# Optimization experiments

Measured on AMD Instinct MI355X. Metric: run time of the kernel, lower is better.

Reference implementation:

```python
import jax, jax.numpy as jnp
import numpy as np

DIM = 256
N_EMBED = 8192
DECAY = 0.99
EPS = 1e-05


def setup_inputs() -> dict:
    key = jax.random.key(0)
    k1, k2, k3, k4 = jax.random.split(key, 4)
    z = jax.random.normal(k1, (16, 32, 32, DIM), dtype=jnp.float32)
    embedding = jax.random.normal(k2, (DIM, N_EMBED), dtype=jnp.float32)
    cluster_size = jax.random.uniform(k3, (N_EMBED,), dtype=jnp.float32)
    embedding_avg = jax.random.normal(k4, (DIM, N_EMBED), dtype=jnp.float32)
    return {"z": z, "embedding": embedding, "cluster_size": cluster_size,
            "embedding_avg": embedding_avg}


def reference(z, embedding, cluster_size, embedding_avg):
    flatten = z.reshape(-1, DIM)  # [N, dim]
    dist = ((flatten ** 2).sum(1, keepdims=True)
            - 2.0 * flatten @ embedding
            + (embedding ** 2).sum(0, keepdims=True))
    embed_ind_flat = jnp.argmin(dist, axis=1)  # [N] int
    embed_ind = embed_ind_flat.reshape(z.shape[:-1])
    # Gather codes: embedding is [dim, n_embed]; quantize [..., dim]
    quantize = jnp.take(embedding.T, embed_ind_flat, axis=0).reshape(z.shape)

    # EMA codebook update (training path), via segment sums (no dense one-hot)
    onehot_sum = jax.ops.segment_sum(
        jnp.ones_like(embed_ind_flat, dtype=flatten.dtype),
        embed_ind_flat, num_segments=N_EMBED)  # [n_embed]
    embed_sum = jax.ops.segment_sum(flatten, embed_ind_flat,
                                    num_segments=N_EMBED).T  # [dim, n_embed]
    new_cluster_size = cluster_size * DECAY + (1.0 - DECAY) * onehot_sum
    new_embedding_avg = embedding_avg * DECAY + (1.0 - DECAY) * embed_sum
    n = new_cluster_size.sum()
    smoothed = (new_cluster_size + EPS) / (n + N_EMBED * EPS) * n
    new_embedding = new_embedding_avg / smoothed[None, :]

    diff = jnp.mean((jax.lax.stop_gradient(quantize) - z) ** 2)
    quantize_st = z + jax.lax.stop_gradient(quantize - z)
    return (quantize_st, diff, embed_ind, new_embedding,
            new_cluster_size, new_embedding_avg)
```

## Files before the change

### kernel.cpp

```cpp
#include <hip/hip_runtime.h>


#define DIMC  256
#define NEMB  8192
#define NROWS 16384

#define OUT_Q      0u
#define OUT_DIFF   4194304u
#define OUT_IDX    4194305u
#define OUT_NEWEMB 4210689u
#define OUT_NEWCS  6307841u
#define OUT_NEWAVG 6316033u

#define WS_EHI    0u
#define WS_ELO    1048576u
#define WS_COUNT  2097152u
#define WS_DIFF   2105344u
#define WS_N      2105345u
#define WS_ENORM  2105346u
#define WS_PACK   2113540u

typedef __attribute__((ext_vector_type(8))) short short8;
typedef __attribute__((ext_vector_type(4))) float f32x4;

__device__ inline void split_bf16(float x, unsigned short& h, unsigned short& l) {
  unsigned u = __float_as_uint(x);
  unsigned r = u + 0x7FFFu + ((u >> 16) & 1u);
  h = (unsigned short)(r >> 16);
  float hf = __uint_as_float((unsigned)h << 16);
  float lo = x - hf;
  unsigned u2 = __float_as_uint(lo);
  unsigned r2 = u2 + 0x7FFFu + ((u2 >> 16) & 1u);
  l = (unsigned short)(r2 >> 16);
}

__device__ inline float bf16_f(unsigned short u) {
  return __uint_as_float((unsigned)u << 16);
}

__global__ __launch_bounds__(256) void prep_kernel(
    const float* __restrict__ z, const float* __restrict__ emb,
    const float* __restrict__ cs, unsigned short* __restrict__ z_hi,
    unsigned short* __restrict__ z_lo, unsigned short* __restrict__ e_hi,
    unsigned short* __restrict__ e_lo, float* __restrict__ enorm,
    float* __restrict__ embsum, unsigned long long* __restrict__ pack,
    float* __restrict__ count_diff, float* __restrict__ n_out) {
  const int b = blockIdx.x;
  const int t = threadIdx.x;
  __shared__ float tile[64][68];
  __shared__ float red[4][64];

  if (b < 1024) {
#pragma unroll
    for (int it = 0; it < 4; ++it) {
      const int idx = (b * 256 + t) + it * 262144;
      const float4 v = reinterpret_cast<const float4*>(z)[idx];
      ushort4 h, l;
      split_bf16(v.x, h.x, l.x);
      split_bf16(v.y, h.y, l.y);
      split_bf16(v.z, h.z, l.z);
      split_bf16(v.w, h.w, l.w);
      reinterpret_cast<ushort4*>(z_hi)[idx] = h;
      reinterpret_cast<ushort4*>(z_lo)[idx] = l;
    }
  } else if (b < 1536) {
    const int bb = b - 1024;
    const int n0 = (bb & 127) * 64;
    const int k0 = (bb >> 7) * 64;
    const int c4 = (t & 15) * 4;
    const int rr = t >> 4;
#pragma unroll
    for (int i = 0; i < 4; ++i) {
      const int kl = rr + i * 16;
      const float4 v = *reinterpret_cast<const float4*>(
          &emb[(size_t)(k0 + kl) * NEMB + n0 + c4]);
      *reinterpret_cast<float4*>(&tile[kl][c4]) = v;
    }
    __syncthreads();
#pragma unroll
    for (int i = 0; i < 4; ++i) {
      const int nr = rr + i * 16;
      float4 v;
      v.x = tile[c4 + 0][nr];
      v.y = tile[c4 + 1][nr];
      v.z = tile[c4 + 2][nr];
      v.w = tile[c4 + 3][nr];
      const size_t off = (size_t)(n0 + nr) * DIMC + k0 + c4;
      ushort4 h, l;
      split_bf16(v.x, h.x, l.x);
      split_bf16(v.y, h.y, l.y);
      split_bf16(v.z, h.z, l.z);
      split_bf16(v.w, h.w, l.w);
      *reinterpret_cast<ushort4*>(&e_hi[off]) = h;
      *reinterpret_cast<ushort4*>(&e_lo[off]) = l;
    }
  } else if (b < 2048) {
    const int bb = b - 1536;
    const float4 zero = {0.f, 0.f, 0.f, 0.f};
#pragma unroll
    for (int it = 0; it < 4; ++it)
      reinterpret_cast<float4*>(embsum)[bb * 1024 + t + it * 256] = zero;
  } else if (b < 2176) {
    const int l = t & 63;
    const int dg = t >> 6;
    const int e = (b - 2048) * 64 + l;
    float s = 0.f;
#pragma unroll 8
    for (int d = dg * 64; d < dg * 64 + 64; ++d) {
      const float v = emb[(size_t)d * NEMB + e];
      s = fmaf(v, v, s);
    }
    red[dg][l] = s;
    __syncthreads();
    if (dg == 0) enorm[e] = red[0][l] + red[1][l] + red[2][l] + red[3][l];
  } else if (b < 2184) {
    const int bb = b - 2176;
    const uint4 ff = {~0u, ~0u, ~0u, ~0u};
#pragma unroll
    for (int it = 0; it < 4; ++it)
      reinterpret_cast<uint4*>(pack)[bb * 1024 + t + it * 256] = ff;
  } else if (b == 2184) {
    for (int i = t; i < 8193; i += 256) count_diff[i] = 0.f;
  } else {
    float s = 0.f;
#pragma unroll
    for (int i = 0; i < 32; ++i) s += cs[t + i * 256];
#pragma unroll
    for (int off = 32; off > 0; off >>= 1) s += __shfl_down(s, off, 64);
    if ((t & 63) == 0) red[0][t >> 6] = s;
    __syncthreads();
    if (t == 0)
      n_out[0] = 0.99f * (red[0][0] + red[0][1] + red[0][2] + red[0][3]) +
                 163.84f;
  }
}

__global__ __launch_bounds__(256, 2) void argmin_mfma_kernel(
    const unsigned short* __restrict__ z_hi, const unsigned short* __restrict__ z_lo,
    const unsigned short* __restrict__ e_hi, const unsigned short* __restrict__ e_lo,
    const float* __restrict__ enorm, unsigned long long* __restrict__ pack) {
  __shared__ short za[16384];
  __shared__ short eb[16384];
  const int tid = threadIdx.x;
  const int bid = blockIdx.x;
  const int r0 = (bid >> 2) * 128;
  const int ebase = (bid & 3) * 2048;
  const int tx = tid & 15;
  const int q = (tid >> 4) & 3;
  const int wave = tid >> 6;
  const int wm = wave & 1;
  const int wn = wave >> 1;

  float rmin[4][4];
  int ridx[4][4];
#pragma unroll
  for (int i = 0; i < 4; ++i)
#pragma unroll
    for (int r = 0; r < 4; ++r) { rmin[i][r] = 3.4028235e38f; ridx[i][r] = 0; }

  for (int nt = 0; nt < 16; ++nt) {
    const int n0 = ebase + nt * 128;
    f32x4 acc[4][4];
#pragma unroll
    for (int i = 0; i < 4; ++i)
#pragma unroll
      for (int j = 0; j < 4; ++j) acc[i][j] = (f32x4)0.0f;

    for (int kt = 0; kt < 4; ++kt) {
      const int k0 = kt * 64;
      __syncthreads();
#pragma unroll
      for (int it = 0; it < 8; ++it) {
        const int P = tid + it * 256;
        const int row = P >> 4;
        const int p = P & 15;
        const int o = (p & 7) ^ (row & 7);
        const unsigned short* zsrc =
            ((p & 8) ? z_lo : z_hi) + (size_t)(r0 + row) * DIMC + k0 + o * 8;
        __builtin_amdgcn_global_load_lds(
            (const __attribute__((address_space(1))) unsigned int*)zsrc,
            (__attribute__((address_space(3))) unsigned int*)&za[P * 8], 16, 0, 0);
        const unsigned short* esrc =
            ((p & 8) ? e_lo : e_hi) + (size_t)(n0 + row) * DIMC + k0 + o * 8;
        __builtin_amdgcn_global_load_lds(
            (const __attribute__((address_space(1))) unsigned int*)esrc,
            (__attribute__((address_space(3))) unsigned int*)&eb[P * 8], 16, 0, 0);
      }
      __syncthreads();
#pragma unroll
      for (int ks = 0; ks < 2; ++ks) {
        short8 ah[4], al[4], bh[4], bl[4];
#pragma unroll
        for (int i = 0; i < 4; ++i) {
          const int rl = wm * 64 + i * 16 + tx;
          const int oa = (ks * 4 + q) ^ (rl & 7);
          ah[i] = *reinterpret_cast<const short8*>(&za[rl * 128 + oa * 8]);
          al[i] = *reinterpret_cast<const short8*>(&za[rl * 128 + (oa + 8) * 8]);
          const int cl = wn * 64 + i * 16 + tx;
          const int ob = (ks * 4 + q) ^ (cl & 7);
          bh[i] = *reinterpret_cast<const short8*>(&eb[cl * 128 + ob * 8]);
          bl[i] = *reinterpret_cast<const short8*>(&eb[cl * 128 + (ob + 8) * 8]);
        }
#pragma unroll
        for (int i = 0; i < 4; ++i)
#pragma unroll
          for (int j = 0; j < 4; ++j) {
            acc[i][j] = __builtin_amdgcn_mfma_f32_16x16x32_bf16(ah[i], bh[j],
                                                               acc[i][j], 0, 0, 0);
            acc[i][j] = __builtin_amdgcn_mfma_f32_16x16x32_bf16(ah[i], bl[j],
                                                               acc[i][j], 0, 0, 0);
            acc[i][j] = __builtin_amdgcn_mfma_f32_16x16x32_bf16(al[i], bh[j],
                                                               acc[i][j], 0, 0, 0);
          }
      }
    }
#pragma unroll
    for (int j = 0; j < 4; ++j) {
      const int col = n0 + wn * 64 + j * 16 + tx;
      const float en = enorm[col];
#pragma unroll
      for (int i = 0; i < 4; ++i)
#pragma unroll
        for (int r = 0; r < 4; ++r) {
          const float s = en - 2.0f * acc[i][j][r];
          if (s < rmin[i][r]) { rmin[i][r] = s; ridx[i][r] = col; }
        }
    }
  }
#pragma unroll
  for (int i = 0; i < 4; ++i)
#pragma unroll
    for (int r = 0; r < 4; ++r) {
      float v = rmin[i][r];
      int ix = ridx[i][r];
#pragma unroll
      for (int off = 1; off < 16; off <<= 1) {
        const float ov = __shfl_xor(v, off, 16);
        const int oi = __shfl_xor(ix, off, 16);
        if (ov < v || (ov == v && oi < ix)) { v = ov; ix = oi; }
      }
      if (tx == 0) {
        const unsigned int fb = __float_as_uint(v);
        const unsigned int sb = (fb & 0x80000000u) ? ~fb : (fb | 0x80000000u);
        const unsigned long long key =
            ((unsigned long long)sb << 13) | (unsigned long long)(unsigned)ix;
        atomicMin(&pack[r0 + wm * 64 + i * 16 + q * 4 + r], key);
      }
    }
}

__global__ __launch_bounds__(256) void gather_update_kernel(
    const float* __restrict__ z, const unsigned short* __restrict__ e_hi,
    const unsigned short* __restrict__ e_lo,
    const unsigned long long* __restrict__ pack, float* __restrict__ out_q,
    float* __restrict__ out_idx, float* __restrict__ embsum,
    float* __restrict__ count, float* __restrict__ diff_acc) {
  const int row = blockIdx.x * 4 + (threadIdx.x >> 6);
  const int lane = threadIdx.x & 63;
  const int e = (int)(pack[row] & 8191ULL);
  if (lane == 0) out_idx[row] = (float)e;
  const float4 zv =
      *reinterpret_cast<const float4*>(&z[(size_t)row * DIMC + lane * 4]);
  const ushort4 h =
      *reinterpret_cast<const ushort4*>(&e_hi[(size_t)e * DIMC + lane * 4]);
  const ushort4 l =
      *reinterpret_cast<const ushort4*>(&e_lo[(size_t)e * DIMC + lane * 4]);
  const float q0 = bf16_f(h.x) + bf16_f(l.x);
  const float q1 = bf16_f(h.y) + bf16_f(l.y);
  const float q2 = bf16_f(h.z) + bf16_f(l.z);
  const float q3 = bf16_f(h.w) + bf16_f(l.w);
  const float d0 = q0 - zv.x, d1 = q1 - zv.y, d2 = q2 - zv.z, d3 = q3 - zv.w;
  float4 st;
  st.x = zv.x + d0; st.y = zv.y + d1; st.z = zv.z + d2; st.w = zv.w + d3;
  *reinterpret_cast<float4*>(&out_q[(size_t)row * DIMC + lane * 4]) = st;

  atomicAdd(&embsum[(size_t)e * DIMC + lane * 4 + 0], zv.x);
  atomicAdd(&embsum[(size_t)e * DIMC + lane * 4 + 1], zv.y);
  atomicAdd(&embsum[(size_t)e * DIMC + lane * 4 + 2], zv.z);
  atomicAdd(&embsum[(size_t)e * DIMC + lane * 4 + 3], zv.w);

  float local = d0 * d0 + d1 * d1 + d2 * d2 + d3 * d3;
#pragma unroll
  for (int off = 32; off > 0; off >>= 1) local += __shfl_down(local, off, 64);

  __shared__ float dred[4];
  if (lane == 0) {
    dred[threadIdx.x >> 6] = local;
    atomicAdd(&count[e], 1.0f);
  }
  __syncthreads();
  if (threadIdx.x == 0)
    atomicAdd(diff_acc, dred[0] + dred[1] + dred[2] + dred[3]);
}

__global__ __launch_bounds__(256) void fin1_kernel(
    const float* __restrict__ eavg, const float* __restrict__ embsum,
    const float* __restrict__ cs, const float* __restrict__ count,
    const float* __restrict__ n_ptr, const float* __restrict__ diff_acc,
    float* __restrict__ out_emb, float* __restrict__ out_ncs,
    float* __restrict__ out_diff) {
  const int b = blockIdx.x;
  const int t = threadIdx.x;
  __shared__ float tile[64][68];
  __shared__ float rs[64];
  if (b < 512) {
    const int e0 = (b & 127) * 64;
    const int d0 = (b >> 7) * 64;
    const int c4 = (t & 15) * 4;
    const int rr = t >> 4;
    if (t < 64) {
      const float n = n_ptr[0];
      const float ncs = cs[e0 + t] * 0.99f + 0.01f * count[e0 + t];
      const float sm = (ncs + 1e-5f) / (n + 0.08192f) * n;
      rs[t] = 1.0f / sm;
    }
#pragma unroll
    for (int i = 0; i < 4; ++i) {
      const int er = rr + i * 16;
      const float4 v = *reinterpret_cast<const float4*>(
          &embsum[(size_t)(e0 + er) * DIMC + d0 + c4]);
      *reinterpret_cast<float4*>(&tile[er][c4]) = v;
    }
    __syncthreads();
#pragma unroll
    for (int i = 0; i < 4; ++i) {
      const int dr = rr + i * 16;
      const size_t g = (size_t)(d0 + dr) * NEMB + e0 + c4;
      const float4 av = *reinterpret_cast<const float4*>(&eavg[g]);
      float4 o;
      o.x = (av.x * 0.99f + 0.01f * tile[c4 + 0][dr]) * rs[c4 + 0];
      o.y = (av.y * 0.99f + 0.01f * tile[c4 + 1][dr]) * rs[c4 + 1];
      o.z = (av.z * 0.99f + 0.01f * tile[c4 + 2][dr]) * rs[c4 + 2];
      o.w = (av.w * 0.99f + 0.01f * tile[c4 + 3][dr]) * rs[c4 + 3];
      *reinterpret_cast<float4*>(&out_emb[g]) = o;
    }
  } else {
    const int g = (b - 512) * 256 + t;
    out_ncs[g] = cs[g] * 0.99f + 0.01f * count[g];
    if (g == 0) out_diff[0] = diff_acc[0] * (1.0f / 4194304.0f);
  }
}

__global__ __launch_bounds__(256) void fin2b_kernel(
    const float* __restrict__ cs, const float* __restrict__ count,
    const float* __restrict__ n_ptr, const float* __restrict__ out_emb,
    float* __restrict__ out_avg) {
  const int g = blockIdx.x * 256 + threadIdx.x;
  const int e = g & 8191;
  const float n = n_ptr[0];
  const float ncs = cs[e] * 0.99f + 0.01f * count[e];
  const float sm = (ncs + 1e-5f) / (n + 0.08192f) * n;
  out_avg[g] = out_emb[g] * sm;
}

extern "C" void kernel_launch(void* const* d_in, const int* in_sizes, int n_in,
                              void* d_out, int out_size, void* d_ws,
                              size_t ws_size, hipStream_t stream) {
  const float* z = (const float*)d_in[0];
  const float* emb = (const float*)d_in[1];
  const float* cs = (const float*)d_in[2];
  const float* eavg = (const float*)d_in[3];
  float* out = (float*)d_out;
  float* ws = (float*)d_ws;

  unsigned short* e_hi = (unsigned short*)(ws + WS_EHI);
  unsigned short* e_lo = (unsigned short*)(ws + WS_ELO);
  float* ws_count = ws + WS_COUNT;
  float* ws_diff = ws + WS_DIFF;
  float* ws_n = ws + WS_N;
  float* ws_enorm = ws + WS_ENORM;
  unsigned long long* ws_pack = (unsigned long long*)(ws + WS_PACK);

  unsigned short* z_hi = (unsigned short*)(out + OUT_Q);
  unsigned short* z_lo = (unsigned short*)(out + OUT_Q + 2097152);
  float* embsum = out + OUT_NEWAVG;

  prep_kernel<<<2186, 256, 0, stream>>>(z, emb, cs, z_hi, z_lo, e_hi, e_lo,
                                        ws_enorm, embsum, ws_pack, ws_count,
                                        ws_n);
  argmin_mfma_kernel<<<512, 256, 0, stream>>>(z_hi, z_lo, e_hi, e_lo, ws_enorm,
                                              ws_pack);
  gather_update_kernel<<<NROWS / 4, 256, 0, stream>>>(
      z, e_hi, e_lo, ws_pack, out + OUT_Q, out + OUT_IDX, embsum, ws_count,
      ws_diff);
  fin1_kernel<<<544, 256, 0, stream>>>(eavg, embsum, cs, ws_count, ws_n,
                                       ws_diff, out + OUT_NEWEMB,
                                       out + OUT_NEWCS, out + OUT_DIFF);
  fin2b_kernel<<<(DIMC * NEMB) / 256, 256, 0, stream>>>(
      cs, ws_count, ws_n, out + OUT_NEWEMB, out + OUT_NEWAVG);
}
```

Baseline: 390.7 us.

## Register-prefetch next tile in argmin GEMM to overlap global loads with MFMA

Replaces the direct global-to-LDS loads in the argmin MFMA kernel with a register-staged software pipeline. The next k/n tile is loaded into registers while the current tile is computed, and address offsets are precomputed once outside the loop. It also raises wave priority around the MFMA block with s_setprio. The intent is to hide global memory latency behind compute, at the cost of 16 extra short8 registers per thread, which may reduce occupancy under launch_bounds(256,2).

```diff
diff --git a/kernel.cpp b/kernel.cpp
--- a/kernel.cpp
+++ b/kernel.cpp
@@ -151,12 +151,36 @@
   const int wm = wave & 1;
   const int wn = wave >> 1;
 
+  const unsigned zdel = (unsigned)(z_lo - z_hi);
+  const unsigned edel = (unsigned)(e_lo - e_hi);
+
+  unsigned zo[8], eo[8];
+#pragma unroll
+  for (int it = 0; it < 8; ++it) {
+    const int P = tid + it * 256;
+    const int row = P >> 4;
+    const int p = P & 15;
+    const int o = (p & 7) ^ (row & 7);
+    zo[it] = ((p & 8) ? zdel : 0u) + (unsigned)(r0 + row) * 256u + (unsigned)o * 8u;
+    eo[it] = ((p & 8) ? edel : 0u) + (unsigned)row * 256u + (unsigned)o * 8u;
+  }
+
   float rmin[4][4];
   int ridx[4][4];
 #pragma unroll
   for (int i = 0; i < 4; ++i)
 #pragma unroll
     for (int r = 0; r < 4; ++r) { rmin[i][r] = 3.4028235e38f; ridx[i][r] = 0; }
+
+  short8 pz[8], pe[8];
+  {
+    const unsigned n00 = (unsigned)ebase * 256u;
+#pragma unroll
+    for (int it = 0; it < 8; ++it) {
+      pz[it] = *reinterpret_cast<const short8*>(z_hi + zo[it]);
+      pe[it] = *reinterpret_cast<const short8*>(e_hi + eo[it] + n00);
+    }
+  }
 
   for (int nt = 0; nt < 16; ++nt) {
     const int n0 = ebase + nt * 128;
@@ -167,26 +191,32 @@
       for (int j = 0; j < 4; ++j) acc[i][j] = (f32x4)0.0f;
 
     for (int kt = 0; kt < 4; ++kt) {
-      const int k0 = kt * 64;
-      __syncthreads();
+      asm volatile("" ::: "memory");
+      __builtin_amdgcn_s_barrier();
+      asm volatile("" ::: "memory");
+
 #pragma unroll
       for (int it = 0; it < 8; ++it) {
-        const int P = tid + it * 256;
-        const int row = P >> 4;
-        const int p = P & 15;
-        const int o = (p & 7) ^ (row & 7);
-        const unsigned short* zsrc =
-            ((p & 8) ? z_lo : z_hi) + (size_t)(r0 + row) * DIMC + k0 + o * 8;
-        __builtin_amdgcn_global_load_lds(
-            (const __attribute__((address_space(1))) unsigned int*)zsrc,
-            (__attribute__((address_space(3))) unsigned int*)&za[P * 8], 16, 0, 0);
-        const unsigned short* esrc =
-            ((p & 8) ? e_lo : e_hi) + (size_t)(n0 + row) * DIMC + k0 + o * 8;
-        __builtin_amdgcn_global_load_lds(
-            (const __attribute__((address_space(1))) unsigned int*)esrc,
-            (__attribute__((address_space(3))) unsigned int*)&eb[P * 8], 16, 0, 0);
+        *reinterpret_cast<short8*>(&za[(tid + it * 256) * 8]) = pz[it];
+        *reinterpret_cast<short8*>(&eb[(tid + it * 256) * 8]) = pe[it];
       }
-      __syncthreads();
+
+      const int s = nt * 4 + kt;
+      if (s < 63) {
+        const int s2 = s + 1;
+        const unsigned k02 = (unsigned)(s2 & 3) * 64u;
+        const unsigned n02 = (unsigned)(ebase + (s2 >> 2) * 128) * 256u + k02;
+#pragma unroll
+        for (int it = 0; it < 8; ++it) {
+          pz[it] = *reinterpret_cast<const short8*>(z_hi + zo[it] + k02);
+          pe[it] = *reinterpret_cast<const short8*>(e_hi + eo[it] + n02);
+        }
+      }
+
+      asm volatile("s_waitcnt lgkmcnt(0)" ::: "memory");
+      __builtin_amdgcn_s_barrier();
+      asm volatile("" ::: "memory");
+
 #pragma unroll
       for (int ks = 0; ks < 2; ++ks) {
         short8 ah[4], al[4], bh[4], bl[4];
@@ -201,6 +231,7 @@
           bh[i] = *reinterpret_cast<const short8*>(&eb[cl * 128 + ob * 8]);
           bl[i] = *reinterpret_cast<const short8*>(&eb[cl * 128 + (ob + 8) * 8]);
         }
+        __builtin_amdgcn_s_setprio(1);
 #pragma unroll
         for (int i = 0; i < 4; ++i)
 #pragma unroll
@@ -212,6 +243,7 @@
             acc[i][j] = __builtin_amdgcn_mfma_f32_16x16x32_bf16(al[i], bh[j],
                                                                acc[i][j], 0, 0, 0);
           }
+        __builtin_amdgcn_s_setprio(0);
       }
     }
 #pragma unroll
```

Result: slower. 438.3 us (+12.2%).

## Double-buffer LDS tiles in argmin MFMA kernel with prefetch of next k-slice

Applied to the files above, without the earlier changes.

Splits the K loop into 32-wide slices and double-buffers the z and codebook tiles in LDS. The next slice's global_load_lds is issued before the MFMAs on the current one, and a single barrier per slice replaces the two syncs per 64-wide chunk. Per-thread source offsets are precomputed once, and the codebook norms are staged into LDS up front so the epilogue avoids global loads. The LDS footprint stays about the same; the risk is that the full vmcnt(0) wait each slice limits how much load latency is actually hidden.

```diff
diff --git a/kernel.cpp b/kernel.cpp
--- a/kernel.cpp
+++ b/kernel.cpp
@@ -141,6 +141,7 @@
     const float* __restrict__ enorm, unsigned long long* __restrict__ pack) {
   __shared__ short za[16384];
   __shared__ short eb[16384];
+  __shared__ float elds[2048];
   const int tid = threadIdx.x;
   const int bid = blockIdx.x;
   const int r0 = (bid >> 2) * 128;
@@ -151,6 +152,38 @@
   const int wm = wave & 1;
   const int wn = wave >> 1;
 
+  const unsigned zdel = (unsigned)(z_lo - z_hi);
+  const unsigned edel = (unsigned)(e_lo - e_hi);
+
+  const int lp = (tid & 7) ^ ((tid >> 3) & 7);
+  const unsigned sz = (lp & 4) ? zdel : 0u;
+  const unsigned se = (lp & 4) ? edel : 0u;
+  const unsigned dch8 = (unsigned)(lp & 3) * 8u;
+  unsigned zo[4], eo[4];
+#pragma unroll
+  for (int it = 0; it < 4; ++it) {
+    const int row_it = (tid >> 3) + it * 32;
+    zo[it] = sz + (unsigned)(r0 + row_it) * 256u + dch8;
+    eo[it] = se + (unsigned)(ebase + row_it) * 256u + dch8;
+  }
+
+  auto STAGE = [&](int sidx) {
+    const unsigned k0s = (unsigned)(sidx & 7) * 32u;
+    const unsigned eas = (unsigned)(sidx >> 3) * 32768u + k0s;
+    const unsigned lb = (unsigned)(sidx & 1) * 8192u + (unsigned)tid * 8u;
+#pragma unroll
+    for (int it = 0; it < 4; ++it) {
+      __builtin_amdgcn_global_load_lds(
+          (const __attribute__((address_space(1))) unsigned int*)(z_hi + zo[it] + k0s),
+          (__attribute__((address_space(3))) unsigned int*)&za[lb + it * 2048],
+          16, 0, 0);
+      __builtin_amdgcn_global_load_lds(
+          (const __attribute__((address_space(1))) unsigned int*)(e_hi + eo[it] + eas),
+          (__attribute__((address_space(3))) unsigned int*)&eb[lb + it * 2048],
+          16, 0, 0);
+    }
+  };
+
   float rmin[4][4];
   int ridx[4][4];
 #pragma unroll
@@ -158,75 +191,73 @@
 #pragma unroll
     for (int r = 0; r < 4; ++r) { rmin[i][r] = 3.4028235e38f; ridx[i][r] = 0; }
 
+  STAGE(0);
+  {
+    const float4 v0 = *reinterpret_cast<const float4*>(&enorm[ebase + tid * 8]);
+    const float4 v1 =
+        *reinterpret_cast<const float4*>(&enorm[ebase + tid * 8 + 4]);
+    *reinterpret_cast<float4*>(&elds[tid * 8]) = v0;
+    *reinterpret_cast<float4*>(&elds[tid * 8 + 4]) = v1;
+  }
+  __syncthreads();
+
   for (int nt = 0; nt < 16; ++nt) {
-    const int n0 = ebase + nt * 128;
     f32x4 acc[4][4];
 #pragma unroll
     for (int i = 0; i < 4; ++i)
 #pragma unroll
       for (int j = 0; j < 4; ++j) acc[i][j] = (f32x4)0.0f;
 
-    for (int kt = 0; kt < 4; ++kt) {
-      const int k0 = kt * 64;
-      __syncthreads();
-#pragma unroll
-      for (int it = 0; it < 8; ++it) {
-        const int P = tid + it * 256;
-        const int row = P >> 4;
-        const int p = P & 15;
-        const int o = (p & 7) ^ (row & 7);
-        const unsigned short* zsrc =
-            ((p & 8) ? z_lo : z_hi) + (size_t)(r0 + row) * DIMC + k0 + o * 8;
-        __builtin_amdgcn_global_load_lds(
-            (const __attribute__((address_space(1))) unsigned int*)zsrc,
-            (__attribute__((address_space(3))) unsigned int*)&za[P * 8], 16, 0, 0);
-        const unsigned short* esrc =
-            ((p & 8) ? e_lo : e_hi) + (size_t)(n0 + row) * DIMC + k0 + o * 8;
-        __builtin_amdgcn_global_load_lds(
-            (const __attribute__((address_space(1))) unsigned int*)esrc,
-            (__attribute__((address_space(3))) unsigned int*)&eb[P * 8], 16, 0, 0);
+    for (int k2 = 0; k2 < 8; ++k2) {
+      const int s = nt * 8 + k2;
+      if (s < 127) STAGE(s + 1);
+
+      const short* zb = &za[(unsigned)(s & 1) * 8192u];
+      const short* ebf = &eb[(unsigned)(s & 1) * 8192u];
+      short8 ah[4], al[4], bh[4], bl[4];
+#pragma unroll
+      for (int i = 0; i < 4; ++i) {
+        const int va = q ^ (tx & 7);
+        const int rl = wm * 64 + i * 16 + tx;
+        ah[i] = *reinterpret_cast<const short8*>(&zb[rl * 64 + va * 8]);
+        al[i] = *reinterpret_cast<const short8*>(&zb[rl * 64 + (va ^ 4) * 8]);
+        const int cl = wn * 64 + i * 16 + tx;
+        bh[i] = *reinterpret_cast<const short8*>(&ebf[cl * 64 + va * 8]);
+        bl[i] = *reinterpret_cast<const short8*>(&ebf[cl * 64 + (va ^ 4) * 8]);
       }
-      __syncthreads();
-#pragma unroll
-      for (int ks = 0; ks < 2; ++ks) {
-        short8 ah[4], al[4], bh[4], bl[4];
-#pragma unroll
-        for (int i = 0; i < 4; ++i) {
-          const int rl = wm * 64 + i * 16 + tx;
-          const int oa = (ks * 4 + q) ^ (rl & 7);
-          ah[i] = *reinterpret_cast<const short8*>(&za[rl * 128 + oa * 8]);
-          al[i] = *reinterpret_cast<const short8*>(&za[rl * 128 + (oa + 8) * 8]);
-          const int cl = wn * 64 + i * 16 + tx;
-          const int ob = (ks * 4 + q) ^ (cl & 7);
-          bh[i] = *reinterpret_cast<const short8*>(&eb[cl * 128 + ob * 8]);
-          bl[i] = *reinterpret_cast<const short8*>(&eb[cl * 128 + (ob + 8) * 8]);
+#pragma unroll
+      for (int i = 0; i < 4; ++i)
+#pragma unroll
+        for (int j = 0; j < 4; ++j) {
+          acc[i][j] = __builtin_amdgcn_mfma_f32_16x16x32_bf16(ah[i], bh[j],
+                                                             acc[i][j], 0, 0, 0);
+          acc[i][j] = __builtin_amdgcn_mfma_f32_16x16x32_bf16(ah[i], bl[j],
+                                                             acc[i][j], 0, 0, 0);
+          acc[i][j] = __builtin_amdgcn_mfma_f32_16x16x32_bf16(al[i], bh[j],
+                                                             acc[i][j], 0, 0, 0);
         }
-#pragma unroll
-        for (int i = 0; i < 4; ++i)
-#pragma unroll
-          for (int j = 0; j < 4; ++j) {
-            acc[i][j] = __builtin_amdgcn_mfma_f32_16x16x32_bf16(ah[i], bh[j],
-                                                               acc[i][j], 0, 0, 0);
-            acc[i][j] = __builtin_amdgcn_mfma_f32_16x16x32_bf16(ah[i], bl[j],
-                                                               acc[i][j], 0, 0, 0);
-            acc[i][j] = __builtin_amdgcn_mfma_f32_16x16x32_bf16(al[i], bh[j],
-                                                               acc[i][j], 0, 0, 0);
-          }
-      }
-    }
+
+      asm volatile("s_waitcnt vmcnt(0) lgkmcnt(0)" ::: "memory");
+      __builtin_amdgcn_sched_barrier(0);
+      __builtin_amdgcn_s_barrier();
+      asm volatile("" ::: "memory");
+    }
+
 #pragma unroll
     for (int j = 0; j < 4; ++j) {
-      const int col = n0 + wn * 64 + j * 16 + tx;
-      const float en = enorm[col];
+      const int cidx = nt * 128 + wn * 64 + j * 16 + tx;
+      const float en = elds[cidx];
+      const int col = ebase + cidx;
 #pragma unroll
       for (int i = 0; i < 4; ++i)
 #pragma unroll
         for (int r = 0; r < 4; ++r) {
-          const float s = en - 2.0f * acc[i][j][r];
-          if (s < rmin[i][r]) { rmin[i][r] = s; ridx[i][r] = col; }
+          const float sc = en - 2.0f * acc[i][j][r];
+          if (sc < rmin[i][r]) { rmin[i][r] = sc; ridx[i][r] = col; }
         }
     }
   }
+
 #pragma unroll
   for (int i = 0; i < 4; ++i)
 #pragma unroll
```

After: 403.2 us. 3.2% more time.

## Replace per-element embsum atomics with per-code row lists and XCD-aware block mapping

Applied to the files above, without the earlier changes.

The gather kernel now appends each row index into a per-code list (capped at 256) instead of doing four float atomicAdds per lane into embsum. A new embsum_kernel sorts each list and sums the listed z rows deterministically, falling back to atomics for overflow. The argmin kernel also remaps block IDs so consecutive row tiles land on the same XCD, aiming for better L2 reuse of the codebook. The cost is an extra kernel launch, a serial insertion sort per code, and lists stored in output scratch space.

```diff
diff --git a/kernel.cpp b/kernel.cpp
--- a/kernel.cpp
+++ b/kernel.cpp
@@ -19,6 +19,8 @@
 #define WS_N      2105345u
 #define WS_ENORM  2105346u
 #define WS_PACK   2113540u
+
+#define LIST_CAP 256
 
 typedef __attribute__((ext_vector_type(8))) short short8;
 typedef __attribute__((ext_vector_type(4))) float f32x4;
@@ -44,7 +46,8 @@
     unsigned short* __restrict__ z_lo, unsigned short* __restrict__ e_hi,
     unsigned short* __restrict__ e_lo, float* __restrict__ enorm,
     float* __restrict__ embsum, unsigned long long* __restrict__ pack,
-    float* __restrict__ count_diff, float* __restrict__ n_out) {
+    float* __restrict__ count_diff, float* __restrict__ n_out,
+    int* __restrict__ cnt_i) {
   const int b = blockIdx.x;
   const int t = threadIdx.x;
   __shared__ float tile[64][68];
@@ -121,6 +124,7 @@
       reinterpret_cast<uint4*>(pack)[bb * 1024 + t + it * 256] = ff;
   } else if (b == 2184) {
     for (int i = t; i < 8193; i += 256) count_diff[i] = 0.f;
+    for (int i = t; i < 8192; i += 256) cnt_i[i] = 0;
   } else {
     float s = 0.f;
 #pragma unroll
@@ -143,8 +147,10 @@
   __shared__ short eb[16384];
   const int tid = threadIdx.x;
   const int bid = blockIdx.x;
-  const int r0 = (bid >> 2) * 128;
-  const int ebase = (bid & 3) * 2048;
+  const int xcd = bid & 7;
+  const int w = bid >> 3;
+  const int r0 = (xcd * 16 + (w & 15)) * 128;
+  const int ebase = (w >> 4) * 2048;
   const int tx = tid & 15;
   const int q = (tid >> 4) & 3;
   const int wave = tid >> 6;
@@ -254,11 +260,18 @@
     const unsigned short* __restrict__ e_lo,
     const unsigned long long* __restrict__ pack, float* __restrict__ out_q,
     float* __restrict__ out_idx, float* __restrict__ embsum,
-    float* __restrict__ count, float* __restrict__ diff_acc) {
+    int* __restrict__ lists, int* __restrict__ cnt_i,
+    float* __restrict__ diff_acc) {
   const int row = blockIdx.x * 4 + (threadIdx.x >> 6);
   const int lane = threadIdx.x & 63;
   const int e = (int)(pack[row] & 8191ULL);
-  if (lane == 0) out_idx[row] = (float)e;
+  int slot = 0;
+  if (lane == 0) {
+    out_idx[row] = (float)e;
+    slot = atomicAdd(&cnt_i[e], 1);
+    if (slot < LIST_CAP) lists[e * LIST_CAP + slot] = row;
+  }
+  slot = __shfl(slot, 0, 64);
   const float4 zv =
       *reinterpret_cast<const float4*>(&z[(size_t)row * DIMC + lane * 4]);
   const ushort4 h =
@@ -274,23 +287,57 @@
   st.x = zv.x + d0; st.y = zv.y + d1; st.z = zv.z + d2; st.w = zv.w + d3;
   *reinterpret_cast<float4*>(&out_q[(size_t)row * DIMC + lane * 4]) = st;
 
-  atomicAdd(&embsum[(size_t)e * DIMC + lane * 4 + 0], zv.x);
-  atomicAdd(&embsum[(size_t)e * DIMC + lane * 4 + 1], zv.y);
-  atomicAdd(&embsum[(size_t)e * DIMC + lane * 4 + 2], zv.z);
-  atomicAdd(&embsum[(size_t)e * DIMC + lane * 4 + 3], zv.w);
+  if (slot >= LIST_CAP) {
+    atomicAdd(&embsum[(size_t)e * DIMC + lane * 4 + 0], zv.x);
+    atomicAdd(&embsum[(size_t)e * DIMC + lane * 4 + 1], zv.y);
+    atomicAdd(&embsum[(size_t)e * DIMC + lane * 4 + 2], zv.z);
+    atomicAdd(&embsum[(size_t)e * DIMC + lane * 4 + 3], zv.w);
+  }
 
   float local = d0 * d0 + d1 * d1 + d2 * d2 + d3 * d3;
 #pragma unroll
   for (int off = 32; off > 0; off >>= 1) local += __shfl_down(local, off, 64);
 
   __shared__ float dred[4];
-  if (lane == 0) {
-    dred[threadIdx.x >> 6] = local;
-    atomicAdd(&count[e], 1.0f);
-  }
+  if (lane == 0) dred[threadIdx.x >> 6] = local;
   __syncthreads();
   if (threadIdx.x == 0)
     atomicAdd(diff_acc, dred[0] + dred[1] + dred[2] + dred[3]);
+}
+
+__global__ __launch_bounds__(256) void embsum_kernel(
+    const float* __restrict__ z, const int* __restrict__ lists,
+    const int* __restrict__ cnt_i, float* __restrict__ embsum,
+    float* __restrict__ count_f) {
+  const int wv = threadIdx.x >> 6;
+  const int lane = threadIdx.x & 63;
+  const int e = blockIdx.x * 4 + wv;
+  __shared__ int sl[4][LIST_CAP];
+  const int n = cnt_i[e];
+  if (lane == 0) count_f[e] = (float)n;
+  const int m = n < LIST_CAP ? n : LIST_CAP;
+  int* myl = sl[wv];
+  for (int i = lane; i < m; i += 64) myl[i] = lists[e * LIST_CAP + i];
+  if (lane == 0) {
+    for (int i = 1; i < m; ++i) {
+      int v = myl[i];
+      int j = i - 1;
+      while (j >= 0 && myl[j] > v) { myl[j + 1] = myl[j]; --j; }
+      myl[j + 1] = v;
+    }
+  }
+  __builtin_amdgcn_wave_barrier();
+  float4 acc = {0.f, 0.f, 0.f, 0.f};
+  for (int i = 0; i < m; ++i) {
+    const int row = myl[i];
+    const float4 v =
+        *reinterpret_cast<const float4*>(&z[(size_t)row * DIMC + lane * 4]);
+    acc.x += v.x; acc.y += v.y; acc.z += v.z; acc.w += v.w;
+  }
+  float4 cur =
+      *reinterpret_cast<const float4*>(&embsum[(size_t)e * DIMC + lane * 4]);
+  cur.x += acc.x; cur.y += acc.y; cur.z += acc.z; cur.w += acc.w;
+  *reinterpret_cast<float4*>(&embsum[(size_t)e * DIMC + lane * 4]) = cur;
 }
 
 __global__ __launch_bounds__(256) void fin1_kernel(
@@ -374,15 +421,19 @@
   unsigned short* z_hi = (unsigned short*)(out + OUT_Q);
   unsigned short* z_lo = (unsigned short*)(out + OUT_Q + 2097152);
   float* embsum = out + OUT_NEWAVG;
+  int* lists = (int*)(out + OUT_NEWEMB);
+  int* cnt_i = (int*)(out + OUT_NEWCS);
 
   prep_kernel<<<2186, 256, 0, stream>>>(z, emb, cs, z_hi, z_lo, e_hi, e_lo,
                                         ws_enorm, embsum, ws_pack, ws_count,
-                                        ws_n);
+                                        ws_n, cnt_i);
   argmin_mfma_kernel<<<512, 256, 0, stream>>>(z_hi, z_lo, e_hi, e_lo, ws_enorm,
                                               ws_pack);
   gather_update_kernel<<<NROWS / 4, 256, 0, stream>>>(
-      z, e_hi, e_lo, ws_pack, out + OUT_Q, out + OUT_IDX, embsum, ws_count,
+      z, e_hi, e_lo, ws_pack, out + OUT_Q, out + OUT_IDX, embsum, lists, cnt_i,
       ws_diff);
+  embsum_kernel<<<NEMB / 4, 256, 0, stream>>>(z, lists, cnt_i, embsum,
+                                              ws_count);
   fin1_kernel<<<544, 256, 0, stream>>>(eavg, embsum, cs, ws_count, ws_n,
                                        ws_diff, out + OUT_NEWEMB,
                                        out + OUT_NEWCS, out + OUT_DIFF);
```

Result: slower. 865.1 us (+121.4%).
